# Optimization experiments

Hardware: AMD Instinct MI355X
Metric: run time of the kernel (lower is better)

## Reference

```python
import jax, jax.numpy as jnp
import numpy as np

H, DK, DV, DEMB = 16, 64, 64, 1024
D_MODEL = H * DV


def setup_inputs() -> dict:
    key = jax.random.key(0)
    ks = jax.random.split(key, 9)
    scale = 0.02
    x = jax.random.normal(ks[0], (4, 2048, DEMB), dtype=jnp.float32)
    wq = jax.random.normal(ks[1], (DEMB, H * DK), dtype=jnp.float32) * scale
    bq = jnp.zeros((H * DK,), dtype=jnp.float32)
    wk = jax.random.normal(ks[2], (DEMB, H * DK), dtype=jnp.float32) * scale
    bk = jnp.zeros((H * DK,), dtype=jnp.float32)
    wv = jax.random.normal(ks[3], (DEMB, H * DV), dtype=jnp.float32) * scale
    bv = jnp.zeros((H * DV,), dtype=jnp.float32)
    wo = jax.random.normal(ks[4], (D_MODEL, D_MODEL), dtype=jnp.float32) * scale
    bo = jnp.zeros((D_MODEL,), dtype=jnp.float32)
    return {"x": x, "wq": wq, "bq": bq, "wk": wk, "bk": bk,
            "wv": wv, "bv": bv, "wo": wo, "bo": bo, "mask": 0}


def _split_heads(t, h):
    # (b, s, h*d) -> (b, h, s, d)
    b, s, _ = t.shape
    return t.reshape(b, s, h, -1).transpose(0, 2, 1, 3)


def reference(x, wq, bq, wk, bk, wv, bv, wo, bo, mask):
    b, s, _ = x.shape
    qs = _split_heads(x @ wq + bq, H)  # (b, h, s, dk)
    ks = _split_heads(x @ wk + bk, H)
    vs = _split_heads(x @ wv + bv, H)  # (b, h, s, dv)
    # FAITHFUL quirk: original scales by 1/sqrt(len(ks[0])) == 1/sqrt(n_heads),
    # not 1/sqrt(d_k).
    scores = jnp.einsum('bhqd,bhkd->bhqk', qs, ks) / jnp.sqrt(jnp.float32(H))
    # FAITHFUL quirk: masked_fill(mask == 0, ...) with scalar bool mask is a
    # no-op (True == 0 is False), so no masking is ever applied.
    attn = jax.nn.softmax(scores, axis=-1)
    out = jnp.einsum('bhqk,bhkd->bhqd', attn, vs)  # (b, h, s, dv)
    out = out.transpose(0, 2, 1, 3).reshape(b, s, D_MODEL)
    return out @ wo + bo
```

## Files before the change

kernel.cpp:

```cpp
#include <hip/hip_runtime.h>
#include <stdint.h>

typedef __attribute__((ext_vector_type(8))) short short8;
typedef __attribute__((ext_vector_type(4))) short short4v;
typedef __attribute__((ext_vector_type(4))) float floatx4;
typedef __attribute__((ext_vector_type(8))) _Float16 half8;
typedef __attribute__((ext_vector_type(2))) __fp16 pk2;

#define SEQ 2048
#define NTOK 8192
#define QSCALE 0.360673760222241f

__device__ __forceinline__ float b2f(unsigned short u){
  union { unsigned int i; float f; } v; v.i = ((unsigned int)u) << 16; return v.f;
}
__device__ __forceinline__ unsigned short f2b(float f){
  union { float f; unsigned int i; } v; v.f = f;
  unsigned int r = v.i + 0x7fffu + ((v.i >> 16) & 1u);
  return (unsigned short)(r >> 16);
}
__device__ __forceinline__ void async16(const unsigned short* g, unsigned short* l){
  __builtin_amdgcn_global_load_lds(
      (const __attribute__((address_space(1))) unsigned int*)g,
      (__attribute__((address_space(3))) unsigned int*)l, 16, 0, 0);
}

__global__ __launch_bounds__(256) void prep_kernel(
    const float* __restrict__ x,
    const float* __restrict__ wq, const float* __restrict__ wk,
    const float* __restrict__ wv, const float* __restrict__ wo,
    const float* __restrict__ bq, const float* __restrict__ bk,
    const float* __restrict__ bv,
    unsigned short* __restrict__ xb,
    unsigned short* __restrict__ wqkvT, unsigned short* __restrict__ woT,
    float* __restrict__ bqkv)
{
  __shared__ unsigned short lT[64][72];
  const int bid = blockIdx.x;
  const int tid = threadIdx.x;
  if (bid < 8192){
    int i = (bid*256 + tid)*4;
    float4 v = *(const float4*)(x + i);
    short4v o;
    o[0] = (short)f2b(v.x); o[1] = (short)f2b(v.y);
    o[2] = (short)f2b(v.z); o[3] = (short)f2b(v.w);
    *(short4v*)(xb + i) = o;
  } else if (bid < 9216){
    int idx = bid - 8192;
    int sel = idx >> 8, rest = idx & 255;
    const float* src = (sel==0)?wq:(sel==1)?wk:(sel==2)?wv:wo;
    unsigned short* dst = (sel<3) ? (wqkvT + (size_t)sel*1024*1024) : woT;
    int n0 = (rest & 15) * 64, k0 = (rest >> 4) * 64;
#pragma unroll
    for (int i=0;i<4;i++){
      int ch = tid + i*256;
      int r = ch>>4, c = (ch&15)*4;
      float4 v = *(const float4*)(src + (size_t)(k0+r)*1024 + n0 + c);
      lT[r][c+0] = f2b(v.x); lT[r][c+1] = f2b(v.y);
      lT[r][c+2] = f2b(v.z); lT[r][c+3] = f2b(v.w);
    }
    __syncthreads();
#pragma unroll
    for (int i=0;i<2;i++){
      int ch = tid + i*256;
      int rn = ch>>3, c = (ch&7)*8;
      short8 v;
#pragma unroll
      for (int j=0;j<8;j++) v[j] = (short)lT[c+j][rn];
      *(short8*)(dst + (size_t)(n0+rn)*1024 + k0 + c) = v;
    }
  } else {
    int i = (bid - 9216)*256 + tid;
    if (i < 3072){
      int sel = i >> 10, j = i & 1023;
      bqkv[i] = (sel==0)?bq[j]:(sel==1)?bk[j]:bv[j];
    }
  }
}

template<int MODE>
__global__ __launch_bounds__(256) void gemm_bt_kernel(
    const unsigned short* __restrict__ A,
    const unsigned short* __restrict__ Bt,
    const float* __restrict__ bias,
    void* __restrict__ Cv,
    unsigned short* __restrict__ Vt,
    int M, int N, int K)
{
  __shared__ unsigned short lA[128*64];
  __shared__ unsigned short lB[128*64];
  const int tid  = threadIdx.x;
  const int lane = tid & 63;
  const int wave = tid >> 6;
  const int quad = lane >> 4;
  const int l15  = lane & 15;
  const int wR = (wave >> 1) * 64;
  const int wC = (wave & 1) * 64;
  const int rowB = blockIdx.y * 128;
  const int colB = blockIdx.x * 128;

  const int srow = wave*32 + (lane>>3);
  const int sc8  = (lane&7) ^ (lane>>3);
  const unsigned short* gA = A  + (size_t)(rowB + srow)*K + sc8*8;
  const unsigned short* gB = Bt + (size_t)(colB + srow)*K + sc8*8;
  unsigned short* lAw = lA + wave*32*64 + lane*8;
  unsigned short* lBw = lB + wave*32*64 + lane*8;

  floatx4 acc[4][4];
#pragma unroll
  for (int t=0;t<4;t++)
#pragma unroll
    for (int u=0;u<4;u++) acc[t][u] = (floatx4){0.f,0.f,0.f,0.f};

  for (int kt = 0; kt < K; kt += 64){
    __syncthreads();
#pragma unroll
    for (int i=0;i<4;i++){
      async16(gA + (size_t)i*8*K + kt, lAw + i*512);
      async16(gB + (size_t)i*8*K + kt, lBw + i*512);
    }
    __syncthreads();
#pragma unroll
    for (int ks=0; ks<2; ks++){
      const int cph = ((ks*4 + quad) ^ (l15 & 7)) * 8;
      short8 af[4], bf[4];
#pragma unroll
      for (int t=0;t<4;t++) af[t] = *(const short8*)&lA[(wR + t*16 + l15)*64 + cph];
#pragma unroll
      for (int u=0;u<4;u++) bf[u] = *(const short8*)&lB[(wC + u*16 + l15)*64 + cph];
#pragma unroll
      for (int t=0;t<4;t++)
#pragma unroll
        for (int u=0;u<4;u++)
          acc[t][u] = __builtin_amdgcn_mfma_f32_16x16x32_bf16(af[t], bf[u], acc[t][u], 0, 0, 0);
    }
  }
  if (MODE == 3 && colB >= 2048){
#pragma unroll
    for (int u=0;u<4;u++){
      int col = colB + wC + u*16 + l15;
      float bval = bias[col];
      int vcol = col - 2048;
      int hh = vcol >> 6, dv = vcol & 63;
#pragma unroll
      for (int t=0;t<4;t++){
        int row0 = rowB + wR + t*16 + quad*4;
        int bb = row0 >> 11, s = row0 & 2047;
        union { pk2 p[2]; short4v s4; } cv;
        cv.p[0] = __builtin_amdgcn_cvt_pkrtz(acc[t][u][0]+bval, acc[t][u][1]+bval);
        cv.p[1] = __builtin_amdgcn_cvt_pkrtz(acc[t][u][2]+bval, acc[t][u][3]+bval);
        *(short4v*)(Vt + ((size_t)(bb*16+hh)*64 + dv)*2048 + s) = cv.s4;
      }
    }
  } else {
#pragma unroll
    for (int u=0;u<4;u++){
      int col = colB + wC + u*16 + l15;
      float bval = bias[col];
      float scale = (MODE == 3 && col < 1024) ? QSCALE : 1.0f;
#pragma unroll
      for (int t=0;t<4;t++){
        int row0 = rowB + wR + t*16 + quad*4;
#pragma unroll
        for (int r=0;r<4;r++){
          float val = (acc[t][u][r] + bval) * scale;
          if (MODE == 1) ((float*)Cv)[(size_t)(row0 + r)*N + col] = val;
          else ((unsigned short*)Cv)[(size_t)(row0 + r)*N + col] = f2b(val);
        }
      }
    }
  }
}

__global__ __launch_bounds__(512) void flash_attn_kernel(
    const unsigned short* __restrict__ qkv,
    const unsigned short* __restrict__ vt,
    unsigned short* __restrict__ attn_out)
{
  __shared__ __align__(16) unsigned short sK [2][128][64];
  __shared__ __align__(16) unsigned short sVt[2][2][64][64];
  const int bh = blockIdx.x;
  const int b = bh >> 4, h = bh & 15;
  const int qt = blockIdx.y;
  const int tid = threadIdx.x;
  const int wave = tid >> 6;
  const int lane = tid & 63;
  const int quad = lane >> 4, l15 = lane & 15;
  const int tok0 = b*SEQ + qt*256;

  short8 qf[2][2];
#pragma unroll
  for (int t=0;t<2;t++)
#pragma unroll
    for (int ks=0;ks<2;ks++)
      qf[t][ks] = *(const short8*)(qkv + (size_t)(tok0 + wave*32 + t*16 + l15)*3072
                                   + h*64 + ks*32 + quad*8);

  floatx4 oacc[2][4];
  floatx4 dacc[2];
#pragma unroll
  for (int t=0;t<2;t++){
    dacc[t] = (floatx4){0.f,0.f,0.f,0.f};
#pragma unroll
    for (int v=0;v<4;v++) oacc[t][v] = (floatx4){0.f,0.f,0.f,0.f};
  }
  const _Float16 one_h = (_Float16)1.0f;
  const half8 ones = {one_h,one_h,one_h,one_h,one_h,one_h,one_h,one_h};

  const unsigned short* kbase[2]; const unsigned short* vbase[2];
  int KD[2], VD[2];
#pragma unroll
  for (int i=0;i<2;i++){
    int c = tid + i*512;
    int kr = c >> 3, kc = c & 7;
    int sr = (kr & 96) | ((kr & 4) << 2) | ((kr >> 1) & 12) | (kr & 3);
    kbase[i] = qkv + (size_t)(b*SEQ + kr)*3072 + 1024 + h*64 + kc*8;
    KD[i] = sr*64 + ((kc ^ (sr & 7)) * 8);
    int dv = c >> 4, vc = c & 15;
    int hfb = vc >> 3, c3 = vc & 7;
    vbase[i] = vt + (size_t)(bh*64 + dv)*2048 + vc*8;
    VD[i] = hfb*4096 + dv*64 + ((c3 ^ (dv & 7)) * 8);
  }
  short8 rk[2], rv[2];
#pragma unroll
  for (int i=0;i<2;i++){
    rk[i] = *(const short8*)(kbase[i]);
    rv[i] = *(const short8*)(vbase[i]);
  }

  for (int it = 0; it < SEQ/128; it++){
    unsigned short* sKb = &sK [it & 1][0][0];
    unsigned short* sVb = &sVt[it & 1][0][0][0];
#pragma unroll
    for (int i=0;i<2;i++){
      *(short8*)(sKb + KD[i]) = rk[i];
      *(short8*)(sVb + VD[i]) = rv[i];
    }
    __syncthreads();
    if (it + 1 < SEQ/128){
      int nx = (it + 1) * 128;
#pragma unroll
      for (int i=0;i<2;i++){
        rk[i] = *(const short8*)(kbase[i] + (size_t)nx*3072);
        rv[i] = *(const short8*)(vbase[i] + nx);
      }
    }

#pragma unroll
    for (int hf=0; hf<2; hf++){
      floatx4 sacc[4][2];
#pragma unroll
      for (int u=0;u<4;u++)
#pragma unroll
        for (int t=0;t<2;t++) sacc[u][t] = (floatx4){0.f,0.f,0.f,0.f};
#pragma unroll
      for (int ks=0;ks<2;ks++){
        short8 kf[4];
#pragma unroll
        for (int u=0;u<4;u++)
          kf[u] = *(const short8*)(sKb + (hf*64 + u*16 + l15)*64
                                   + ((ks*4 + quad) ^ (l15 & 7)) * 8);
#pragma unroll
        for (int u=0;u<4;u++)
#pragma unroll
          for (int t=0;t<2;t++)
            sacc[u][t] = __builtin_amdgcn_mfma_f32_16x16x32_bf16(kf[u], qf[t][ks], sacc[u][t], 0,0,0);
      }

      unsigned pw[4][2][2];
#pragma unroll
      for (int t=0;t<2;t++){
#pragma unroll
        for (int u=0;u<4;u++){
          float p0 = __builtin_amdgcn_exp2f(sacc[u][t][0]);
          float p1 = __builtin_amdgcn_exp2f(sacc[u][t][1]);
          float p2 = __builtin_amdgcn_exp2f(sacc[u][t][2]);
          float p3 = __builtin_amdgcn_exp2f(sacc[u][t][3]);
          union { pk2 p; unsigned u32; } c0, c1;
          c0.p = __builtin_amdgcn_cvt_pkrtz(p0,p1);
          c1.p = __builtin_amdgcn_cvt_pkrtz(p2,p3);
          pw[u][t][0] = c0.u32; pw[u][t][1] = c1.u32;
        }
      }
      half8 pf[2][2];
#pragma unroll
      for (int t=0;t<2;t++)
#pragma unroll
        for (int B=0;B<2;B++){
          union { unsigned u32[4]; half8 h; } a;
          a.u32[0] = pw[2*B  ][t][0]; a.u32[1] = pw[2*B  ][t][1];
          a.u32[2] = pw[2*B+1][t][0]; a.u32[3] = pw[2*B+1][t][1];
          pf[t][B] = a.h;
        }

#pragma unroll
      for (int t=0;t<2;t++)
#pragma unroll
        for (int B=0;B<2;B++)
          dacc[t] = __builtin_amdgcn_mfma_f32_16x16x32_f16(pf[t][B], ones, dacc[t], 0,0,0);

#pragma unroll
      for (int v=0;v<4;v++){
#pragma unroll
        for (int B=0;B<2;B++){
          union { short8 s; half8 h; } vb;
          vb.s = *(const short8*)(sVb + hf*4096 + (v*16 + l15)*64
                                  + ((B*4 + quad) ^ (l15 & 7)) * 8);
#pragma unroll
          for (int t=0;t<2;t++)
            oacc[t][v] = __builtin_amdgcn_mfma_f32_16x16x32_f16(pf[t][B], vb.h, oacc[t][v], 0,0,0);
        }
      }
    }
  }

#pragma unroll
  for (int t=0;t<2;t++){
#pragma unroll
    for (int r=0;r<4;r++){
      float inv = 1.0f / dacc[t][r];
      int tok = tok0 + wave*32 + t*16 + quad*4 + r;
#pragma unroll
      for (int v=0;v<4;v++)
        attn_out[(size_t)tok*1024 + h*64 + v*16 + l15] = f2b(oacc[t][v][r] * inv);
    }
  }
}

extern "C" void kernel_launch(void* const* d_in, const int* in_sizes, int n_in,
                              void* d_out, int out_size, void* d_ws, size_t ws_size,
                              hipStream_t stream)
{
  const float* x  = (const float*)d_in[0];
  const float* wq = (const float*)d_in[1];
  const float* bq = (const float*)d_in[2];
  const float* wk = (const float*)d_in[3];
  const float* bk = (const float*)d_in[4];
  const float* wv = (const float*)d_in[5];
  const float* bv = (const float*)d_in[6];
  const float* wo = (const float*)d_in[7];
  const float* bo = (const float*)d_in[8];
  float* out = (float*)d_out;

  char* ws = (char*)d_ws;
  unsigned short* wqkvT  = (unsigned short*)(ws);
  unsigned short* woT    = (unsigned short*)(ws + 6291456);
  float*          bqkv   = (float*)(ws + 8388608);
  unsigned short* xb     = (unsigned short*)(ws + 8400896);
  unsigned short* qkvbuf = (unsigned short*)(ws + 25178112);
  unsigned short* vtbuf  = (unsigned short*)(ws + 75509760);
  unsigned short* aobuf  = (unsigned short*)(ws + 92286976);

  prep_kernel<<<dim3(9228), 256, 0, stream>>>(x, wq, wk, wv, wo, bq, bk, bv,
                                              xb, wqkvT, woT, bqkv);
  gemm_bt_kernel<3><<<dim3(24, 64), 256, 0, stream>>>(xb, wqkvT, bqkv, qkvbuf, vtbuf,
                                                      8192, 3072, 1024);
  flash_attn_kernel<<<dim3(64, 8), 512, 0, stream>>>(qkvbuf, vtbuf, aobuf);
  gemm_bt_kernel<1><<<dim3(8, 64), 256, 0, stream>>>(aobuf, woT, bo, out, nullptr,
                                                     8192, 1024, 1024);
}
```

Before: 271.9 us.

## Triple-buffer GEMM LDS tiles with async prefetch and K-step of 32

Replaces the GEMM main loop, which used two barriers and one 64-wide K tile per iteration, with a three-stage ring of 32-wide LDS buffers. Global-to-LDS async loads for step t+2 are issued before the MFMAs of step t, and a single vmcnt wait plus barrier separates steps. This is meant to hide global load latency behind matrix math. The LDS layout is also repacked so that two rows share a 64-element LDS row, with a new swizzle. In exchange the loop runs twice as many barrier steps, and the packed layout must keep the MFMA fragment mapping correct for the existing epilogue.

New measurement: 288.2 us. 6.0% more time.

```diff
diff --git a/kernel.cpp b/kernel.cpp
--- a/kernel.cpp
+++ b/kernel.cpp
@@ -87,54 +87,87 @@
     unsigned short* __restrict__ Vt,
     int M, int N, int K)
 {
-  __shared__ unsigned short lA[128*64];
-  __shared__ unsigned short lB[128*64];
+  __shared__ unsigned short lAf[3*4096];
+  __shared__ unsigned short lBf[3*4096];
   const int tid  = threadIdx.x;
   const int lane = tid & 63;
   const int wave = tid >> 6;
   const int quad = lane >> 4;
   const int l15  = lane & 15;
+  const int wR2 = (wave >> 1) * 32;
+  const int wC2 = (wave & 1) * 32;
+  const int rowB = blockIdx.y * 128;
+  const int colB = blockIdx.x * 128;
+
+  const int cl = (lane & 7) ^ ((lane >> 3) & 7);
+  const int r0 = wave*16 + (lane >> 3);
+  const unsigned short* srcA0 = A  + (size_t)(rowB + 2*r0 + (cl>>2))*K + (cl&3)*8;
+  const unsigned short* srcB0 = Bt + (size_t)(colB + 2*r0 + (cl>>2))*K + (cl&3)*8;
+  const unsigned short* srcA1 = srcA0 + (size_t)16*K;
+  const unsigned short* srcB1 = srcB0 + (size_t)16*K;
+  const int dstoff = wave*1024 + lane*8;
+
+  const int l15h = l15 >> 1;
+  const int cph  = (((l15 & 1) << 2) | quad) ^ l15h;
+
+  floatx4 acc[4][4];
+#pragma unroll
+  for (int t=0;t<4;t++)
+#pragma unroll
+    for (int u=0;u<4;u++) acc[t][u] = (floatx4){0.f,0.f,0.f,0.f};
+
+#define GEMM_ISSUE(BUFIDX, KOFF)                                   \
+  {                                                                \
+    unsigned short* dA = lAf + (BUFIDX)*4096 + dstoff;             \
+    unsigned short* dB = lBf + (BUFIDX)*4096 + dstoff;             \
+    async16(srcA0 + (KOFF), dA);                                   \
+    async16(srcA1 + (KOFF), dA + 512);                             \
+    async16(srcB0 + (KOFF), dB);                                   \
+    async16(srcB1 + (KOFF), dB + 512);                             \
+  }
+
+#define GEMM_STEP(BUFIDX)                                          \
+  {                                                                \
+    const unsigned short* sA = lAf + (BUFIDX)*4096;                \
+    const unsigned short* sB = lBf + (BUFIDX)*4096;                \
+    short8 af[4], bf[4];                                           \
+    _Pragma("unroll")                                              \
+    for (int t=0;t<4;t++)                                          \
+      af[t] = *(const short8*)(sA + (wR2 + t*8 + l15h)*64 + cph*8);\
+    _Pragma("unroll")                                              \
+    for (int u=0;u<4;u++)                                          \
+      bf[u] = *(const short8*)(sB + (wC2 + u*8 + l15h)*64 + cph*8);\
+    _Pragma("unroll")                                              \
+    for (int t=0;t<4;t++)                                          \
+      _Pragma("unroll")                                            \
+      for (int u=0;u<4;u++)                                        \
+        acc[t][u] = __builtin_amdgcn_mfma_f32_16x16x32_bf16(       \
+            af[t], bf[u], acc[t][u], 0, 0, 0);                     \
+  }
+
+  const int nsteps = K >> 5;
+  GEMM_ISSUE(0, 0)
+  GEMM_ISSUE(1, 32)
+  asm volatile("s_waitcnt vmcnt(4)\n\ts_barrier" ::: "memory");
+
+  int cur = 0, nxt = 2;
+  for (int t = 0; t < nsteps - 2; ++t){
+    GEMM_ISSUE(nxt, (t+2)*32)
+    GEMM_STEP(cur)
+    asm volatile("s_waitcnt vmcnt(4)\n\ts_barrier" ::: "memory");
+    cur = (cur == 2) ? 0 : cur + 1;
+    nxt = (nxt == 2) ? 0 : nxt + 1;
+  }
+  GEMM_STEP(cur)
+  asm volatile("s_waitcnt vmcnt(0)\n\ts_barrier" ::: "memory");
+  cur = (cur == 2) ? 0 : cur + 1;
+  GEMM_STEP(cur)
+
+#undef GEMM_ISSUE
+#undef GEMM_STEP
+
   const int wR = (wave >> 1) * 64;
   const int wC = (wave & 1) * 64;
-  const int rowB = blockIdx.y * 128;
-  const int colB = blockIdx.x * 128;
-
-  const int srow = wave*32 + (lane>>3);
-  const int sc8  = (lane&7) ^ (lane>>3);
-  const unsigned short* gA = A  + (size_t)(rowB + srow)*K + sc8*8;
-  const unsigned short* gB = Bt + (size_t)(colB + srow)*K + sc8*8;
-  unsigned short* lAw = lA + wave*32*64 + lane*8;
-  unsigned short* lBw = lB + wave*32*64 + lane*8;
-
-  floatx4 acc[4][4];
-#pragma unroll
-  for (int t=0;t<4;t++)
-#pragma unroll
-    for (int u=0;u<4;u++) acc[t][u] = (floatx4){0.f,0.f,0.f,0.f};
-
-  for (int kt = 0; kt < K; kt += 64){
-    __syncthreads();
-#pragma unroll
-    for (int i=0;i<4;i++){
-      async16(gA + (size_t)i*8*K + kt, lAw + i*512);
-      async16(gB + (size_t)i*8*K + kt, lBw + i*512);
-    }
-    __syncthreads();
-#pragma unroll
-    for (int ks=0; ks<2; ks++){
-      const int cph = ((ks*4 + quad) ^ (l15 & 7)) * 8;
-      short8 af[4], bf[4];
-#pragma unroll
-      for (int t=0;t<4;t++) af[t] = *(const short8*)&lA[(wR + t*16 + l15)*64 + cph];
-#pragma unroll
-      for (int u=0;u<4;u++) bf[u] = *(const short8*)&lB[(wC + u*16 + l15)*64 + cph];
-#pragma unroll
-      for (int t=0;t<4;t++)
-#pragma unroll
-        for (int u=0;u<4;u++)
-          acc[t][u] = __builtin_amdgcn_mfma_f32_16x16x32_bf16(af[t], bf[u], acc[t][u], 0, 0, 0);
-    }
-  }
   if (MODE == 3 && colB >= 2048){
 #pragma unroll
     for (int u=0;u<4;u++){
```
